# Kernel tuning notes

Measured on AMD Instinct MI355X. Metric: run time of the kernel, lower is better.

Reference implementation:

```python
import jax, jax.numpy as jnp
import numpy as np

MIN_NORM = 1e-15
MARGIN = 9.0
N_ENT, N_REL, DIM = 200000, 500, 64
B, NC = 1024, 1024


def expmap0(u):
    # Poincare ball (c=1) exponential map at origin: tanh(|u|) * u / |u|
    un = jnp.maximum(jnp.linalg.norm(u, axis=-1, keepdims=True), MIN_NORM)
    return jnp.tanh(un) * u / un


def mobius_add(x, y):
    x2 = jnp.sum(x * x, -1, keepdims=True)
    y2 = jnp.sum(y * y, -1, keepdims=True)
    xy = jnp.sum(x * y, -1, keepdims=True)
    num = (1.0 + 2.0 * xy + y2) * x + (1.0 - x2) * y
    den = 1.0 + 2.0 * xy + x2 * y2
    return num / jnp.maximum(den, MIN_NORM)


def givens_rotations(r, x):
    # r, x: [..., D], D even. Rotate consecutive coordinate pairs of x by
    # the normalized 2-vectors of r (cos=g0, sin=g1).
    shp = x.shape
    g = r.reshape(shp[:-1] + (-1, 2))
    g = g / jnp.maximum(jnp.linalg.norm(g, axis=-1, keepdims=True), MIN_NORM)
    xp = x.reshape(shp[:-1] + (-1, 2))
    out = jnp.stack(
        [g[..., 0] * xp[..., 0] - g[..., 1] * xp[..., 1],
         g[..., 1] * xp[..., 0] + g[..., 0] * xp[..., 1]], axis=-1)
    return out.reshape(shp)


def busemann_distance(x, p):
    # B_p(x) = log(|p - x|^2 / (1 - |x|^2)); broadcasts over leading dims
    num = jnp.sum((p - x) ** 2, axis=-1)
    den = 1.0 - jnp.sum(x * x, axis=-1)
    return jnp.log(jnp.maximum(num, MIN_NORM) / jnp.maximum(den, MIN_NORM))


def setup_inputs() -> dict:
    key = jax.random.key(0)
    ks = jax.random.split(key, 9)
    init = 0.001
    return {
        "u_idx": jax.random.randint(ks[0], (B,), 0, N_ENT),
        "r_idx": jax.random.randint(ks[1], (B,), 0, N_REL),
        "v_idx": jax.random.randint(ks[2], (B, NC), 0, N_ENT),
        "emb_entity": init * jax.random.normal(ks[3], (N_ENT, DIM), jnp.float32),
        "rel_diag": 2.0 * jax.random.uniform(ks[4], (N_REL, DIM), jnp.float32) - 1.0,
        "relation_bias_1": init * jax.random.normal(ks[5], (N_REL, DIM), jnp.float32),
        "relation_bias_2": init * jax.random.normal(ks[6], (N_REL, DIM), jnp.float32),
        "bias_head": jnp.zeros((N_ENT,), jnp.float32),
        "bias_tail": jnp.zeros((N_ENT,), jnp.float32),
        "sigma": jax.random.uniform(ks[7], (N_REL,), jnp.float32),
    }


def reference(u_idx, r_idx, v_idx, emb_entity, rel_diag,
              relation_bias_1, relation_bias_2, bias_head, bias_tail, sigma):
    head = expmap0(emb_entity[u_idx])            # [B, D]
    tail = expmap0(emb_entity[v_idx])            # [B, N, D]
    r_b1 = expmap0(relation_bias_1[r_idx])       # [B, D]
    r_b2 = expmap0(relation_bias_2[r_idx])       # [B, D]
    r_d = rel_diag[r_idx]                        # [B, D]

    head = mobius_add(head, r_b1)
    head = givens_rotations(r_d, head)
    head = mobius_add(head, r_b2)                # [B, D]

    head_b = head[:, None, :]                    # broadcast over candidates
    dist_tail = busemann_distance(tail, head_b)  # [B, N]
    dist_head = busemann_distance(head_b, tail)  # [B, N]

    sig = jax.nn.sigmoid(sigma[r_idx])[:, None]  # [B, 1]
    dist = sig * dist_tail + (1.0 - sig) * dist_head
    neg_dist = MARGIN - dist
    return neg_dist + bias_head[u_idx][:, None] + bias_tail[v_idx]
```

## Files before the change

kernel.cpp:

```cpp
#include <hip/hip_runtime.h>

#define MIN_NORM 1e-15f
#define MARGIN 9.0f
#define DIM 64
#define B_ROWS 1024
#define NC 1024

__device__ inline float wave_reduce_sum(float v) {
    #pragma unroll
    for (int off = 32; off > 0; off >>= 1) v += __shfl_xor(v, off, 64);
    return v;
}

__global__ __launch_bounds__(256) void head_kernel(
    const int* __restrict__ u_idx, const int* __restrict__ r_idx,
    const float* __restrict__ emb, const float* __restrict__ rel_diag,
    const float* __restrict__ rb1, const float* __restrict__ rb2,
    const float* __restrict__ bias_head, const float* __restrict__ sigma,
    float* __restrict__ head_out, float* __restrict__ scal_out)
{
    const int lane = threadIdx.x & 63;
    const int row = blockIdx.x * 4 + (threadIdx.x >> 6);
    if (row >= B_ROWS) return;
    const int u = u_idx[row];
    const int r = r_idx[row];

    float x = emb[(long)u * DIM + lane];
    {
        float n2 = wave_reduce_sum(x * x);
        float un = fmaxf(sqrtf(n2), MIN_NORM);
        x = tanhf(un) / un * x;
    }
    float y = rb1[(long)r * DIM + lane];
    {
        float n2 = wave_reduce_sum(y * y);
        float un = fmaxf(sqrtf(n2), MIN_NORM);
        y = tanhf(un) / un * y;
    }
    {
        float x2 = wave_reduce_sum(x * x);
        float y2 = wave_reduce_sum(y * y);
        float xy = wave_reduce_sum(x * y);
        float den = 1.0f + 2.0f * xy + x2 * y2;
        x = ((1.0f + 2.0f * xy + y2) * x + (1.0f - x2) * y) / fmaxf(den, MIN_NORM);
    }
    {
        float g  = rel_diag[(long)r * DIM + lane];
        float go = __shfl_xor(g, 1, 64);
        float xo = __shfl_xor(x, 1, 64);
        float gn = fmaxf(sqrtf(g * g + go * go), MIN_NORM);
        x = ((lane & 1) ? (g * xo + go * x) : (g * x - go * xo)) / gn;
    }
    float z = rb2[(long)r * DIM + lane];
    {
        float n2 = wave_reduce_sum(z * z);
        float un = fmaxf(sqrtf(n2), MIN_NORM);
        z = tanhf(un) / un * z;
    }
    {
        float x2 = wave_reduce_sum(x * x);
        float y2 = wave_reduce_sum(z * z);
        float xy = wave_reduce_sum(x * z);
        float den = 1.0f + 2.0f * xy + x2 * y2;
        x = ((1.0f + 2.0f * xy + y2) * x + (1.0f - x2) * z) / fmaxf(den, MIN_NORM);
    }
    float h2 = wave_reduce_sum(x * x);
    head_out[(long)row * DIM + lane] = x;
    if (lane == 0) {
        scal_out[row * 4 + 0] = h2;
        scal_out[row * 4 + 1] = logf(fmaxf(1.0f - h2, MIN_NORM));
        scal_out[row * 4 + 2] = 1.0f / (1.0f + expf(-sigma[r]));
        scal_out[row * 4 + 3] = bias_head[u];
    }
}

__global__ __launch_bounds__(256) void score_kernel(
    const int* __restrict__ v_idx, const float* __restrict__ emb,
    const float* __restrict__ bias_tail,
    const float* __restrict__ head, const float* __restrict__ scal,
    float* __restrict__ out)
{
    const int b = blockIdx.y;
    const int base = blockIdx.x * 256;
    const int t = threadIdx.x;
    const int g = t >> 2;
    const int sub = t & 3;

    __shared__ float4 sh[DIM / 4];
    __shared__ float ss[4];
    if (t < DIM / 4)
        sh[t] = ((const float4*)(head + (long)b * DIM))[t];
    if (t < 4)
        ss[t] = scal[b * 4 + t];

    const int4 v4 = ((const int4*)(v_idx + (long)b * NC + base))[g];
    const int v0 = v4.x, v1 = v4.y, v2 = v4.z, v3 = v4.w;

    __syncthreads();

    float4 h[4];
    #pragma unroll
    for (int k = 0; k < 4; ++k) h[k] = sh[4 * k + sub];

    float4 e[4][4];
    {
        const float4* p0 = (const float4*)(emb + (long)v0 * DIM);
        const float4* p1 = (const float4*)(emb + (long)v1 * DIM);
        const float4* p2 = (const float4*)(emb + (long)v2 * DIM);
        const float4* p3 = (const float4*)(emb + (long)v3 * DIM);
        #pragma unroll
        for (int k = 0; k < 4; ++k) {
            e[0][k] = p0[4 * k + sub];
            e[1][k] = p1[4 * k + sub];
            e[2][k] = p2[4 * k + sub];
            e[3][k] = p3[4 * k + sub];
        }
    }

    float dot[4], e2[4];
    #pragma unroll
    for (int j = 0; j < 4; ++j) {
        float d = 0.0f, q = 0.0f;
        #pragma unroll
        for (int k = 0; k < 4; ++k) {
            float4 ee = e[j][k];
            float4 hh = h[k];
            d = fmaf(hh.x, ee.x, d); d = fmaf(hh.y, ee.y, d);
            d = fmaf(hh.z, ee.z, d); d = fmaf(hh.w, ee.w, d);
            q = fmaf(ee.x, ee.x, q); q = fmaf(ee.y, ee.y, q);
            q = fmaf(ee.z, ee.z, q); q = fmaf(ee.w, ee.w, q);
        }
        d += __shfl_xor(d, 1, 64); d += __shfl_xor(d, 2, 64);
        q += __shfl_xor(q, 1, 64); q += __shfl_xor(q, 2, 64);
        dot[j] = d; e2[j] = q;
    }

    const float D  = (sub == 0) ? dot[0] : (sub == 1) ? dot[1] : (sub == 2) ? dot[2] : dot[3];
    const float E  = (sub == 0) ? e2[0]  : (sub == 1) ? e2[1]  : (sub == 2) ? e2[2]  : e2[3];
    const int myv  = (sub == 0) ? v0     : (sub == 1) ? v1     : (sub == 2) ? v2     : v3;

    const float h2 = ss[0], ldh = ss[1], sig = ss[2], bh = ss[3];
    const float un = fmaxf(sqrtf(E), MIN_NORM);
    const float tn = tanhf(un);
    const float s = tn / un;
    const float t2 = tn * tn;
    const float num = h2 + t2 - 2.0f * s * D;
    const float dist = logf(fmaxf(num, MIN_NORM))
                     - sig * logf(fmaxf(1.0f - t2, MIN_NORM))
                     - (1.0f - sig) * ldh;
    out[(long)b * NC + base + t] = MARGIN - dist + bh + bias_tail[myv];
}

extern "C" void kernel_launch(void* const* d_in, const int* in_sizes, int n_in,
                              void* d_out, int out_size, void* d_ws, size_t ws_size,
                              hipStream_t stream) {
    const int*   u_idx     = (const int*)d_in[0];
    const int*   r_idx     = (const int*)d_in[1];
    const int*   v_idx     = (const int*)d_in[2];
    const float* emb       = (const float*)d_in[3];
    const float* rel_diag  = (const float*)d_in[4];
    const float* rb1       = (const float*)d_in[5];
    const float* rb2       = (const float*)d_in[6];
    const float* bias_head = (const float*)d_in[7];
    const float* bias_tail = (const float*)d_in[8];
    const float* sigma     = (const float*)d_in[9];

    float* head = (float*)d_ws;
    float* scal = head + (long)B_ROWS * DIM;

    head_kernel<<<B_ROWS / 4, 256, 0, stream>>>(
        u_idx, r_idx, emb, rel_diag, rb1, rb2, bias_head, sigma, head, scal);

    score_kernel<<<dim3(NC / 256, B_ROWS), 256, 0, stream>>>(
        v_idx, emb, bias_tail, head, scal, (float*)d_out);
}
```

Before: 139.5 us.

## Precompute bf16 tail embeddings and per-entity scalars to shrink gather traffic

Adds a pre-pass over all 200k entities that applies expmap0, stores the mapped rows as packed bf16, and stores per-entity |t|^2, log(1-|t|^2) and bias_tail. The score kernel then gathers 128-byte bf16 rows plus one float4 instead of 256-byte fp32 rows, and no longer computes tanh or norms per candidate. The trade is a full-table conversion pass on every call (about 51MB read), the extra escal gather, and bf16 rounding error in the dot product. The old fp32 path is kept as a fallback when the workspace is too small.

```diff
diff --git a/kernel.cpp b/kernel.cpp
--- a/kernel.cpp
+++ b/kernel.cpp
@@ -1,16 +1,24 @@
 #include <hip/hip_runtime.h>
+#include <stdint.h>
 
 #define MIN_NORM 1e-15f
 #define MARGIN 9.0f
 #define DIM 64
 #define B_ROWS 1024
 #define NC 1024
+#define N_ENT 200000
 
 __device__ inline float wave_reduce_sum(float v) {
     #pragma unroll
     for (int off = 32; off > 0; off >>= 1) v += __shfl_xor(v, off, 64);
     return v;
 }
+
+__device__ inline uint32_t f2bf_bits(float x) {
+    uint32_t u = __float_as_uint(x);
+    return (u + 0x7fffu + ((u >> 16) & 1u)) >> 16;
+}
+__device__ inline float bfbits2f(uint32_t b) { return __uint_as_float(b << 16); }
 
 __global__ __launch_bounds__(256) void head_kernel(
     const int* __restrict__ u_idx, const int* __restrict__ r_idx,
@@ -74,7 +82,120 @@
     }
 }
 
-__global__ __launch_bounds__(256) void score_kernel(
+__global__ __launch_bounds__(256) void convert_kernel(
+    const float* __restrict__ emb, const float* __restrict__ bias_tail,
+    uint32_t* __restrict__ tau, float4* __restrict__ escal)
+{
+    const int t = threadIdx.x;
+    const int g = t >> 2, sub = t & 3;
+    const long row = (long)blockIdx.x * 64 + g;
+    if (row >= N_ENT) return;
+
+    const float4* p = (const float4*)(emb + row * DIM);
+    float4 c[4];
+    #pragma unroll
+    for (int k = 0; k < 4; ++k) c[k] = p[sub + 4 * k];
+
+    float n2 = 0.0f;
+    #pragma unroll
+    for (int k = 0; k < 4; ++k) {
+        n2 = fmaf(c[k].x, c[k].x, n2); n2 = fmaf(c[k].y, c[k].y, n2);
+        n2 = fmaf(c[k].z, c[k].z, n2); n2 = fmaf(c[k].w, c[k].w, n2);
+    }
+    n2 += __shfl_xor(n2, 1, 64); n2 += __shfl_xor(n2, 2, 64);
+    const float un = fmaxf(sqrtf(n2), MIN_NORM);
+    const float s = tanhf(un) / un;
+
+    float t2 = 0.0f;
+    uint32_t* trow = tau + row * 32;
+    #pragma unroll
+    for (int k = 0; k < 4; ++k) {
+        const int ci = sub + 4 * k;
+        uint32_t b0 = f2bf_bits(s * c[k].x), b1 = f2bf_bits(s * c[k].y);
+        uint32_t b2 = f2bf_bits(s * c[k].z), b3 = f2bf_bits(s * c[k].w);
+        float r0 = bfbits2f(b0), r1 = bfbits2f(b1), r2 = bfbits2f(b2), r3 = bfbits2f(b3);
+        t2 = fmaf(r0, r0, t2); t2 = fmaf(r1, r1, t2);
+        t2 = fmaf(r2, r2, t2); t2 = fmaf(r3, r3, t2);
+        uint2 packed = make_uint2(b0 | (b1 << 16), b2 | (b3 << 16));
+        ((uint2*)trow)[ci] = packed;
+    }
+    t2 += __shfl_xor(t2, 1, 64); t2 += __shfl_xor(t2, 2, 64);
+    if (sub == 0) {
+        float lt = logf(fmaxf(1.0f - t2, MIN_NORM));
+        escal[row] = make_float4(t2, lt, bias_tail[row], 0.0f);
+    }
+}
+
+__global__ __launch_bounds__(256) void score_bf16_kernel(
+    const int* __restrict__ v_idx, const uint32_t* __restrict__ tau,
+    const float4* __restrict__ escal,
+    const float* __restrict__ head, const float* __restrict__ scal,
+    float* __restrict__ out)
+{
+    const int b = blockIdx.y;
+    const int base = blockIdx.x * 256;
+    const int t = threadIdx.x;
+    const int g = t >> 2, sub = t & 3;
+
+    __shared__ float4 sh[DIM / 4];
+    __shared__ float ss[4];
+    if (t < DIM / 4) sh[t] = ((const float4*)(head + (long)b * DIM))[t];
+    if (t < 4) ss[t] = scal[b * 4 + t];
+
+    const int4 v4 = ((const int4*)(v_idx + (long)b * NC + base))[g];
+    const int vv[4] = {v4.x, v4.y, v4.z, v4.w};
+
+    __syncthreads();
+
+    const float4 hA = sh[2 * sub], hB = sh[2 * sub + 1];
+    const float4 hC = sh[8 + 2 * sub], hD = sh[9 + 2 * sub];
+
+    uint4 q0[4], q1[4];
+    #pragma unroll
+    for (int j = 0; j < 4; ++j) {
+        const uint32_t* r = tau + (long)vv[j] * 32;
+        q0[j] = ((const uint4*)r)[sub];
+        q1[j] = ((const uint4*)r)[4 + sub];
+    }
+
+    float dot[4];
+    #pragma unroll
+    for (int j = 0; j < 4; ++j) {
+        float d = 0.0f;
+        uint4 a = q0[j], bq = q1[j];
+        d = fmaf(hA.x, bfbits2f(a.x & 0xffffu), d);
+        d = fmaf(hA.y, bfbits2f(a.x >> 16), d);
+        d = fmaf(hA.z, bfbits2f(a.y & 0xffffu), d);
+        d = fmaf(hA.w, bfbits2f(a.y >> 16), d);
+        d = fmaf(hB.x, bfbits2f(a.z & 0xffffu), d);
+        d = fmaf(hB.y, bfbits2f(a.z >> 16), d);
+        d = fmaf(hB.z, bfbits2f(a.w & 0xffffu), d);
+        d = fmaf(hB.w, bfbits2f(a.w >> 16), d);
+        d = fmaf(hC.x, bfbits2f(bq.x & 0xffffu), d);
+        d = fmaf(hC.y, bfbits2f(bq.x >> 16), d);
+        d = fmaf(hC.z, bfbits2f(bq.y & 0xffffu), d);
+        d = fmaf(hC.w, bfbits2f(bq.y >> 16), d);
+        d = fmaf(hD.x, bfbits2f(bq.z & 0xffffu), d);
+        d = fmaf(hD.y, bfbits2f(bq.z >> 16), d);
+        d = fmaf(hD.z, bfbits2f(bq.w & 0xffffu), d);
+        d = fmaf(hD.w, bfbits2f(bq.w >> 16), d);
+        d += __shfl_xor(d, 1, 64);
+        d += __shfl_xor(d, 2, 64);
+        dot[j] = d;
+    }
+
+    const float D = (sub == 0) ? dot[0] : (sub == 1) ? dot[1] : (sub == 2) ? dot[2] : dot[3];
+    const int myv = vv[sub];
+    const float4 es = escal[myv];
+
+    const float h2 = ss[0], ldh = ss[1], sig = ss[2], bh = ss[3];
+    const float num = h2 + es.x - 2.0f * D;
+    const float dist = logf(fmaxf(num, MIN_NORM))
+                     - sig * es.y - (1.0f - sig) * ldh;
+    out[(long)b * NC + base + t] = MARGIN - dist + bh + es.z;
+}
+
+__global__ __launch_bounds__(256) void score_fp32_kernel(
     const int* __restrict__ v_idx, const float* __restrict__ emb,
     const float* __restrict__ bias_tail,
     const float* __restrict__ head, const float* __restrict__ scal,
@@ -83,19 +204,15 @@
     const int b = blockIdx.y;
     const int base = blockIdx.x * 256;
     const int t = threadIdx.x;
-    const int g = t >> 2;
-    const int sub = t & 3;
+    const int g = t >> 2, sub = t & 3;
 
     __shared__ float4 sh[DIM / 4];
     __shared__ float ss[4];
-    if (t < DIM / 4)
-        sh[t] = ((const float4*)(head + (long)b * DIM))[t];
-    if (t < 4)
-        ss[t] = scal[b * 4 + t];
+    if (t < DIM / 4) sh[t] = ((const float4*)(head + (long)b * DIM))[t];
+    if (t < 4) ss[t] = scal[b * 4 + t];
 
     const int4 v4 = ((const int4*)(v_idx + (long)b * NC + base))[g];
     const int v0 = v4.x, v1 = v4.y, v2 = v4.z, v3 = v4.w;
-
     __syncthreads();
 
     float4 h[4];
@@ -123,8 +240,7 @@
         float d = 0.0f, q = 0.0f;
         #pragma unroll
         for (int k = 0; k < 4; ++k) {
-            float4 ee = e[j][k];
-            float4 hh = h[k];
+            float4 ee = e[j][k]; float4 hh = h[k];
             d = fmaf(hh.x, ee.x, d); d = fmaf(hh.y, ee.y, d);
             d = fmaf(hh.z, ee.z, d); d = fmaf(hh.w, ee.w, d);
             q = fmaf(ee.x, ee.x, q); q = fmaf(ee.y, ee.y, q);
@@ -165,12 +281,22 @@
     const float* bias_tail = (const float*)d_in[8];
     const float* sigma     = (const float*)d_in[9];
 
-    float* head = (float*)d_ws;
-    float* scal = head + (long)B_ROWS * DIM;
+    char* ws = (char*)d_ws;
+    float*    head  = (float*)ws;
+    float*    scal  = (float*)(ws + 262144);
+    uint32_t* tau   = (uint32_t*)(ws + 278528);
+    float4*   escal = (float4*)(ws + 278528 + (size_t)N_ENT * 128);
+    const size_t need = 278528 + (size_t)N_ENT * 128 + (size_t)N_ENT * 16;
 
     head_kernel<<<B_ROWS / 4, 256, 0, stream>>>(
         u_idx, r_idx, emb, rel_diag, rb1, rb2, bias_head, sigma, head, scal);
 
-    score_kernel<<<dim3(NC / 256, B_ROWS), 256, 0, stream>>>(
-        v_idx, emb, bias_tail, head, scal, (float*)d_out);
-}
+    if (ws_size >= need) {
+        convert_kernel<<<(N_ENT + 63) / 64, 256, 0, stream>>>(emb, bias_tail, tau, escal);
+        score_bf16_kernel<<<dim3(NC / 256, B_ROWS), 256, 0, stream>>>(
+            v_idx, tau, escal, head, scal, (float*)d_out);
+    } else {
+        score_fp32_kernel<<<dim3(NC / 256, B_ROWS), 256, 0, stream>>>(
+            v_idx, emb, bias_tail, head, scal, (float*)d_out);
+    }
+}
```

Measured after the change: 140.4 us. Within noise of the previous version (+0.7%).
